# Kernel tuning notes

Hardware: AMD Instinct MI355X
Metric: run time of the kernel (lower is better)

Reference implementation:

```python
import jax, jax.numpy as jnp
import numpy as np


def _proj(W, b, x):
    # 1x1 conv == per-pixel GEMM over channels: [O,C] x [B,C,H,W] -> [B,O,H,W]
    return jnp.einsum('oc,bchw->bohw', W, x) + b[None, :, None, None]


def _cross(src, ctx, Wq, bq, Wk, bk, Wv, bv):
    # queries from src, keys/values from ctx; returns [B,C,H,W]
    B, C, H, W = src.shape
    HW = H * W
    q = _proj(Wq, bq, src).reshape(B, -1, HW)   # [B, C//8, HW]
    k = _proj(Wk, bk, ctx).reshape(B, -1, HW)   # [B, C//8, HW]
    v = _proj(Wv, bv, ctx).reshape(B, C, HW)    # [B, C,    HW]
    # attn[b,i,j] = softmax_j( q[b,:,i] . k[b,:,j] )
    attn = jax.nn.softmax(jnp.einsum('bci,bcj->bij', q, k), axis=-1)
    out = jnp.einsum('bcj,bij->bci', v, attn)   # [B, C, HW]
    return out.reshape(B, C, H, W)


def setup_inputs() -> dict:
    key = jax.random.key(0)
    ks = jax.random.split(key, 8)
    dim = 256
    B, H, W = 4, 64, 64
    return {
        'x': jax.random.normal(ks[0], (B, dim, H, W), jnp.float32),
        'y': jax.random.normal(ks[1], (B, dim, H, W), jnp.float32),
        'Wq': jax.random.normal(ks[2], (dim // 8, dim), jnp.float32) * 0.05,
        'bq': jax.random.normal(ks[3], (dim // 8,), jnp.float32) * 0.05,
        'Wk': jax.random.normal(ks[4], (dim // 8, dim), jnp.float32) * 0.05,
        'bk': jax.random.normal(ks[5], (dim // 8,), jnp.float32) * 0.05,
        'Wv': jax.random.normal(ks[6], (dim, dim), jnp.float32) * 0.05,
        'bv': jax.random.normal(ks[7], (dim,), jnp.float32) * 0.05,
    }


def reference(x, y, Wq, bq, Wk, bk, Wv, bv):
    outx = _cross(x, y, Wq, bq, Wk, bk, Wv, bv)  # x queries attend to y
    outy = _cross(y, x, Wq, bq, Wk, bk, Wv, bv)  # y queries attend to x
    return (outx, outy)
```

## Files before the change

### kernel.cpp

```cpp
#include <hip/hip_runtime.h>

#define BB 4
#define CC 256
#define DD 32
#define SS 4096

typedef __bf16 bf16;
typedef __bf16 bf16x8 __attribute__((ext_vector_type(8)));
typedef __bf16 bf16x4 __attribute__((ext_vector_type(4)));
typedef float f32x4 __attribute__((ext_vector_type(4)));
typedef unsigned int u32;
typedef unsigned short u16;

#define Q_OFF  0
#define K_OFF  1048576
#define V_OFF  2097152
#define WB_OFF 10485760

static __device__ __forceinline__ u32 pack2(float lo, float hi) {
    bf16 a = (bf16)lo, b = (bf16)hi;
    u16 ua = __builtin_bit_cast(u16, a), ub = __builtin_bit_cast(u16, b);
    return (u32)ua | ((u32)ub << 16);
}

__global__ __launch_bounds__(256) void convert_w_kernel(
    const float* __restrict__ Wq, const float* __restrict__ Wk,
    const float* __restrict__ Wv, bf16* __restrict__ wb)
{
    const int gid = blockIdx.x*256 + threadIdx.x;
    const int idx = gid*8;
    const int o = idx >> 8, cc = idx & 255;
    const float* row = (o < 32) ? (Wq + (size_t)o*CC)
                     : (o < 64) ? (Wk + (size_t)(o-32)*CC)
                                : (Wv + (size_t)(o-64)*CC);
    const float4 a = *(const float4*)(row + cc);
    const float4 c = *(const float4*)(row + cc + 4);
    bf16x8 pk;
    pk[0]=(bf16)a.x; pk[1]=(bf16)a.y; pk[2]=(bf16)a.z; pk[3]=(bf16)a.w;
    pk[4]=(bf16)c.x; pk[5]=(bf16)c.y; pk[6]=(bf16)c.z; pk[7]=(bf16)c.w;
    *(bf16x8*)(wb + idx) = pk;
}

__global__ __launch_bounds__(256, 2) void proj_all_kernel(
    const float* __restrict__ x, const float* __restrict__ y,
    const bf16* __restrict__ wb,
    const float* __restrict__ bq, const float* __restrict__ bk,
    const float* __restrict__ bv,
    bf16* __restrict__ qout, bf16* __restrict__ kout, bf16* __restrict__ vout)
{
    __shared__ __align__(16) char smem[2*5120];
    bf16* xT  = (bf16*)smem;
    u32*  xTw = (u32*)smem;

    const int t    = threadIdx.x;
    const int lane = t & 63;
    const int w    = t >> 6;
    const int ln   = lane & 15;
    const int quad = lane >> 4;

    const int bid  = blockIdx.x;
    const int dirb = bid & 7;
    const int src  = dirb >> 2;
    const int b    = dirb & 3;
    const int i0   = (bid >> 3) * 64;
    const float* in = src ? y : x;
    const float* xbase = in + (size_t)b*CC*SS + i0;

    const int cp = t >> 4;
    const int pq = (t & 15) * 4;

    float bias[5];
    #pragma unroll
    for (int nbl = 0; nbl < 5; ++nbl) {
        const int o = 80*w + nbl*16 + ln;
        bias[nbl] = (o < 32) ? bq[o] : (o < 64) ? bk[o-32] : bv[o-64];
    }
    f32x4 acc[4][5];
    #pragma unroll
    for (int mb = 0; mb < 4; ++mb)
        #pragma unroll
        for (int nbl = 0; nbl < 5; ++nbl)
            acc[mb][nbl] = (f32x4){bias[nbl], bias[nbl], bias[nbl], bias[nbl]};

    const bf16* wrow = wb + (size_t)(80*w + ln)*CC + quad*8;
    bf16x8 bf[5];
    #pragma unroll
    for (int nbl = 0; nbl < 5; ++nbl)
        bf[nbl] = *(const bf16x8*)(wrow + (size_t)nbl*16*CC);

    {
        const float* r0 = xbase + (size_t)(2*cp)*SS + pq;
        const float4 a0 = *(const float4*)r0;
        const float4 a1 = *(const float4*)(r0 + SS);
        xTw[(pq+0)*20 + cp] = pack2(a0.x, a1.x);
        xTw[(pq+1)*20 + cp] = pack2(a0.y, a1.y);
        xTw[(pq+2)*20 + cp] = pack2(a0.z, a1.z);
        xTw[(pq+3)*20 + cp] = pack2(a0.w, a1.w);
    }
    float4 a0, a1;
    {
        const float* r1 = xbase + (size_t)(32 + 2*cp)*SS + pq;
        a0 = *(const float4*)r1;
        a1 = *(const float4*)(r1 + SS);
    }
    __syncthreads();

    for (int n = 0; n < 8; ++n) {
        bf16x8 af[4];
        #pragma unroll
        for (int mb = 0; mb < 4; ++mb)
            af[mb] = *(const bf16x8*)(xT + (n&1)*2560 + (mb*16 + ln)*40 + quad*8);
        if (n < 7) {
            u32* dst = xTw + ((n+1)&1)*1280;
            dst[(pq+0)*20 + cp] = pack2(a0.x, a1.x);
            dst[(pq+1)*20 + cp] = pack2(a0.y, a1.y);
            dst[(pq+2)*20 + cp] = pack2(a0.z, a1.z);
            dst[(pq+3)*20 + cp] = pack2(a0.w, a1.w);
        }
        {
            const int cc2 = ((n+2)*32) & 255;
            const float* r2 = xbase + (size_t)(cc2 + 2*cp)*SS + pq;
            a0 = *(const float4*)r2;
            a1 = *(const float4*)(r2 + SS);
        }
        #pragma unroll
        for (int mb = 0; mb < 4; ++mb)
            #pragma unroll
            for (int nbl = 0; nbl < 5; ++nbl)
                acc[mb][nbl] = __builtin_amdgcn_mfma_f32_16x16x32_bf16(
                                   af[mb], bf[nbl], acc[mb][nbl], 0, 0, 0);
        const int ccn = ((n+1)*32) & 255;
        #pragma unroll
        for (int nbl = 0; nbl < 5; ++nbl)
            bf[nbl] = *(const bf16x8*)(wrow + (size_t)nbl*16*CC + ccn);
        __syncthreads();
    }

    bf16* qo = qout + (size_t)(src*BB + b)*SS*DD;
    bf16* ko = kout + (size_t)(src*BB + b)*SS*DD;
    bf16* vo = vout + (size_t)(src*BB + b)*CC*SS;
    #pragma unroll
    for (int nbl = 0; nbl < 5; ++nbl) {
        const int o = 80*w + nbl*16 + ln;
        if (o < 32) {
            #pragma unroll
            for (int mb = 0; mb < 4; ++mb)
                #pragma unroll
                for (int r = 0; r < 4; ++r)
                    qo[(size_t)(i0 + mb*16 + quad*4 + r)*DD + o] = (bf16)acc[mb][nbl][r];
        } else if (o < 64) {
            #pragma unroll
            for (int mb = 0; mb < 4; ++mb)
                #pragma unroll
                for (int r = 0; r < 4; ++r)
                    ko[(size_t)(i0 + mb*16 + quad*4 + r)*DD + (o-32)] = (bf16)acc[mb][nbl][r];
        } else {
            const int c = o - 64;
            #pragma unroll
            for (int mb = 0; mb < 4; ++mb) {
                bf16x4 pk;
                #pragma unroll
                for (int r = 0; r < 4; ++r) pk[r] = (bf16)acc[mb][nbl][r];
                *(bf16x4*)(vo + (size_t)c*SS + i0 + mb*16 + quad*4) = pk;
            }
        }
    }
}

#define SM_M 16.0f

__global__ __launch_bounds__(256, 2) void attn_kernel(
    const bf16* __restrict__ qg, const bf16* __restrict__ kg,
    const bf16* __restrict__ vg, float* __restrict__ out)
{
    __shared__ __align__(16) char smem[18688];
    bf16*  p_s = (bf16*)smem;
    float* l_s = (float*)(smem + 18432);

    const int t    = threadIdx.x;
    const int lane = t & 63;
    const int w    = t >> 6;
    const int ln   = lane & 15;
    const int quad = lane >> 4;

    const int bid  = blockIdx.x;
    const int dirb = bid & 7;
    const int dir  = dirb >> 2;
    const int b    = dirb & 3;
    const int i0   = (bid >> 3) * 64;

    const bf16* q = qg + ((size_t)dir*BB + b)*SS*DD + (size_t)i0*DD;
    const bf16* k = kg + ((size_t)(1-dir)*BB + b)*SS*DD;
    const bf16* v = vg + ((size_t)(1-dir)*BB + b)*CC*SS;
    float* op = out + ((size_t)dir*BB + b)*CC*SS;

    const bf16x8 b_q = *(const bf16x8*)(q + (size_t)(w*16 + ln)*DD + quad*8);
    const bf16* kbase = k + (size_t)ln*DD + quad*8;
    const bf16* vptr[4];
    #pragma unroll
    for (int cb = 0; cb < 4; ++cb)
        vptr[cb] = v + (size_t)(w*64 + cb*16 + ln)*SS + quad*8;

    f32x4 o[4][4];
    #pragma unroll
    for (int qb = 0; qb < 4; ++qb)
        #pragma unroll
        for (int cb = 0; cb < 4; ++cb) o[qb][cb] = (f32x4){0.f,0.f,0.f,0.f};
    float lp = 0.f;

    bf16x8 kf[4], vf[2][4];
    #pragma unroll
    for (int nb = 0; nb < 4; ++nb)
        kf[nb] = *(const bf16x8*)(kbase + (size_t)(nb*16)*DD);
    #pragma unroll
    for (int ks = 0; ks < 2; ++ks)
        #pragma unroll
        for (int cb = 0; cb < 4; ++cb)
            vf[ks][cb] = *(const bf16x8*)(vptr[cb] + ks*32);

    {
        f32x4 s[4];
        #pragma unroll
        for (int nb = 0; nb < 4; ++nb)
            s[nb] = __builtin_amdgcn_mfma_f32_16x16x32_bf16(
                        kf[nb], b_q, (f32x4){0.f,0.f,0.f,0.f}, 0, 0, 0);
        #pragma unroll
        for (int nb = 0; nb < 4; ++nb)
            kf[nb] = *(const bf16x8*)(kbase + (size_t)(64 + nb*16)*DD);
        #pragma unroll
        for (int nb = 0; nb < 4; ++nb) {
            bf16x4 pk;
            #pragma unroll
            for (int r = 0; r < 4; ++r) {
                const float e = __expf(fminf(s[nb][r] - SM_M, 60.0f));
                lp += e;
                pk[r] = (bf16)e;
            }
            *(bf16x4*)(p_s + (w*16 + ln)*72 + nb*16 + quad*4) = pk;
        }
    }

    for (int n = 0; n < 64; ++n) {
        __syncthreads();
        const bf16* pr = p_s + (n & 1)*4608;
        bf16* pw = p_s + ((n + 1) & 1)*4608;

        f32x4 s[4];
        if (n < 63) {
            #pragma unroll
            for (int nb = 0; nb < 4; ++nb)
                s[nb] = __builtin_amdgcn_mfma_f32_16x16x32_bf16(
                            kf[nb], b_q, (f32x4){0.f,0.f,0.f,0.f}, 0, 0, 0);
            const int j2 = ((n + 2) << 6) & (SS - 1);
            #pragma unroll
            for (int nb = 0; nb < 4; ++nb)
                kf[nb] = *(const bf16x8*)(kbase + (size_t)(j2 + nb*16)*DD);
        }

        #pragma unroll
        for (int ks = 0; ks < 2; ++ks) {
            bf16x8 ap[4];
            #pragma unroll
            for (int qb = 0; qb < 4; ++qb)
                ap[qb] = *(const bf16x8*)(pr + (qb*16 + ln)*72 + ks*32 + quad*8);
            #pragma unroll
            for (int qb = 0; qb < 4; ++qb)
                #pragma unroll
                for (int cb = 0; cb < 4; ++cb)
                    o[qb][cb] = __builtin_amdgcn_mfma_f32_16x16x32_bf16(
                                    ap[qb], vf[ks][cb], o[qb][cb], 0, 0, 0);
        }
        const int j1 = ((n + 1) << 6) & (SS - 1);
        #pragma unroll
        for (int ks = 0; ks < 2; ++ks)
            #pragma unroll
            for (int cb = 0; cb < 4; ++cb)
                vf[ks][cb] = *(const bf16x8*)(vptr[cb] + j1 + ks*32);

        if (n < 63) {
            #pragma unroll
            for (int nb = 0; nb < 4; ++nb) {
                bf16x4 pk;
                #pragma unroll
                for (int r = 0; r < 4; ++r) {
                    const float e = __expf(fminf(s[nb][r] - SM_M, 60.0f));
                    lp += e;
                    pk[r] = (bf16)e;
                }
                *(bf16x4*)(pw + (w*16 + ln)*72 + nb*16 + quad*4) = pk;
            }
        }
    }

    lp += __shfl_xor(lp, 16);
    lp += __shfl_xor(lp, 32);
    if (lane < 16) l_s[w*16 + ln] = lp;
    __syncthreads();

    #pragma unroll
    for (int qb = 0; qb < 4; ++qb) {
        const f32x4 lq = *(const f32x4*)(l_s + qb*16 + quad*4);
        const float ri0 = 1.0f/lq[0], ri1 = 1.0f/lq[1], ri2 = 1.0f/lq[2], ri3 = 1.0f/lq[3];
        #pragma unroll
        for (int cb = 0; cb < 4; ++cb) {
            const int c = w*64 + cb*16 + ln;
            float4 val = make_float4(o[qb][cb][0]*ri0, o[qb][cb][1]*ri1,
                                     o[qb][cb][2]*ri2, o[qb][cb][3]*ri3);
            *(float4*)(op + (size_t)c*SS + i0 + qb*16 + quad*4) = val;
        }
    }
}

extern "C" void kernel_launch(void* const* d_in, const int* in_sizes, int n_in,
                              void* d_out, int out_size, void* d_ws, size_t ws_size,
                              hipStream_t stream)
{
    const float* x  = (const float*)d_in[0];
    const float* y  = (const float*)d_in[1];
    const float* Wq = (const float*)d_in[2];
    const float* bq = (const float*)d_in[3];
    const float* Wk = (const float*)d_in[4];
    const float* bk = (const float*)d_in[5];
    const float* Wv = (const float*)d_in[6];
    const float* bv = (const float*)d_in[7];
    float* out = (float*)d_out;
    bf16* ws   = (bf16*)d_ws;

    bf16* qw = ws + Q_OFF;
    bf16* kw = ws + K_OFF;
    bf16* vw = ws + V_OFF;
    bf16* wb = ws + WB_OFF;

    convert_w_kernel<<<40,  256, 0, stream>>>(Wq, Wk, Wv, wb);
    proj_all_kernel <<<512, 256, 0, stream>>>(x, y, wb, bq, bk, bv, qw, kw, vw);
    attn_kernel     <<<512, 256, 0, stream>>>(qw, kw, vw, out);
}
```

Before: 253.6 us.

## Halve projection tile, swizzle LDS, and deepen attention K/V prefetch pipeline

The projection kernel now processes 32 pixels per block, so twice as many blocks launch and occupancy rises to four blocks per CU. Only half the threads stage input, and an XOR-swizzled LDS layout replaces the padded one. The attention kernel also swaps its padded P tile for an XOR-swizzled layout to avoid bank conflicts. It double-buffers K and V fragments in registers, prefetching one more iteration ahead and unrolling by two. This raises register pressure and reuses less weight data per pixel in the projection.

```diff
diff --git a/kernel.cpp b/kernel.cpp
--- a/kernel.cpp
+++ b/kernel.cpp
@@ -41,14 +41,14 @@
     *(bf16x8*)(wb + idx) = pk;
 }
 
-__global__ __launch_bounds__(256, 2) void proj_all_kernel(
+__global__ __launch_bounds__(256, 4) void proj_all_kernel(
     const float* __restrict__ x, const float* __restrict__ y,
     const bf16* __restrict__ wb,
     const float* __restrict__ bq, const float* __restrict__ bk,
     const float* __restrict__ bv,
     bf16* __restrict__ qout, bf16* __restrict__ kout, bf16* __restrict__ vout)
 {
-    __shared__ __align__(16) char smem[2*5120];
+    __shared__ __align__(16) char smem[2*4096];
     bf16* xT  = (bf16*)smem;
     u32*  xTw = (u32*)smem;
 
@@ -62,12 +62,13 @@
     const int dirb = bid & 7;
     const int src  = dirb >> 2;
     const int b    = dirb & 3;
-    const int i0   = (bid >> 3) * 64;
+    const int i0   = (bid >> 3) * 32;
     const float* in = src ? y : x;
     const float* xbase = in + (size_t)b*CC*SS + i0;
 
-    const int cp = t >> 4;
-    const int pq = (t & 15) * 4;
+    const bool stager = (t < 128);
+    const int cp = t >> 3;
+    const int pq = (t & 7) * 4;
 
     float bias[5];
     #pragma unroll
@@ -75,9 +76,9 @@
         const int o = 80*w + nbl*16 + ln;
         bias[nbl] = (o < 32) ? bq[o] : (o < 64) ? bk[o-32] : bv[o-64];
     }
-    f32x4 acc[4][5];
-    #pragma unroll
-    for (int mb = 0; mb < 4; ++mb)
+    f32x4 acc[2][5];
+    #pragma unroll
+    for (int mb = 0; mb < 2; ++mb)
         #pragma unroll
         for (int nbl = 0; nbl < 5; ++nbl)
             acc[mb][nbl] = (f32x4){bias[nbl], bias[nbl], bias[nbl], bias[nbl]};
@@ -88,43 +89,45 @@
     for (int nbl = 0; nbl < 5; ++nbl)
         bf[nbl] = *(const bf16x8*)(wrow + (size_t)nbl*16*CC);
 
-    {
+    float4 a0, a1;
+    if (stager) {
         const float* r0 = xbase + (size_t)(2*cp)*SS + pq;
-        const float4 a0 = *(const float4*)r0;
-        const float4 a1 = *(const float4*)(r0 + SS);
-        xTw[(pq+0)*20 + cp] = pack2(a0.x, a1.x);
-        xTw[(pq+1)*20 + cp] = pack2(a0.y, a1.y);
-        xTw[(pq+2)*20 + cp] = pack2(a0.z, a1.z);
-        xTw[(pq+3)*20 + cp] = pack2(a0.w, a1.w);
-    }
-    float4 a0, a1;
-    {
+        const float4 c0 = *(const float4*)r0;
+        const float4 c1 = *(const float4*)(r0 + SS);
+        const int chb = cp >> 2, lo = cp & 3;
+        xTw[(pq+0)*32 + ((chb ^ ((pq+0)&7)) << 2) + lo] = pack2(c0.x, c1.x);
+        xTw[(pq+1)*32 + ((chb ^ ((pq+1)&7)) << 2) + lo] = pack2(c0.y, c1.y);
+        xTw[(pq+2)*32 + ((chb ^ ((pq+2)&7)) << 2) + lo] = pack2(c0.z, c1.z);
+        xTw[(pq+3)*32 + ((chb ^ ((pq+3)&7)) << 2) + lo] = pack2(c0.w, c1.w);
         const float* r1 = xbase + (size_t)(32 + 2*cp)*SS + pq;
         a0 = *(const float4*)r1;
         a1 = *(const float4*)(r1 + SS);
     }
     __syncthreads();
 
+    const int swz = ln & 7;
     for (int n = 0; n < 8; ++n) {
-        bf16x8 af[4];
-        #pragma unroll
-        for (int mb = 0; mb < 4; ++mb)
-            af[mb] = *(const bf16x8*)(xT + (n&1)*2560 + (mb*16 + ln)*40 + quad*8);
-        if (n < 7) {
-            u32* dst = xTw + ((n+1)&1)*1280;
-            dst[(pq+0)*20 + cp] = pack2(a0.x, a1.x);
-            dst[(pq+1)*20 + cp] = pack2(a0.y, a1.y);
-            dst[(pq+2)*20 + cp] = pack2(a0.z, a1.z);
-            dst[(pq+3)*20 + cp] = pack2(a0.w, a1.w);
-        }
-        {
+        bf16x8 af[2];
+        #pragma unroll
+        for (int mb = 0; mb < 2; ++mb)
+            af[mb] = *(const bf16x8*)(xT + (n&1)*2048 + (mb*16 + ln)*64
+                                      + ((quad ^ swz) << 3));
+        if (n < 7 && stager) {
+            u32* dst = xTw + ((n+1)&1)*1024;
+            const int chb = cp >> 2, lo = cp & 3;
+            dst[(pq+0)*32 + ((chb ^ ((pq+0)&7)) << 2) + lo] = pack2(a0.x, a1.x);
+            dst[(pq+1)*32 + ((chb ^ ((pq+1)&7)) << 2) + lo] = pack2(a0.y, a1.y);
+            dst[(pq+2)*32 + ((chb ^ ((pq+2)&7)) << 2) + lo] = pack2(a0.z, a1.z);
+            dst[(pq+3)*32 + ((chb ^ ((pq+3)&7)) << 2) + lo] = pack2(a0.w, a1.w);
+        }
+        if (stager) {
             const int cc2 = ((n+2)*32) & 255;
             const float* r2 = xbase + (size_t)(cc2 + 2*cp)*SS + pq;
             a0 = *(const float4*)r2;
             a1 = *(const float4*)(r2 + SS);
         }
         #pragma unroll
-        for (int mb = 0; mb < 4; ++mb)
+        for (int mb = 0; mb < 2; ++mb)
             #pragma unroll
             for (int nbl = 0; nbl < 5; ++nbl)
                 acc[mb][nbl] = __builtin_amdgcn_mfma_f32_16x16x32_bf16(
@@ -144,20 +147,20 @@
         const int o = 80*w + nbl*16 + ln;
         if (o < 32) {
             #pragma unroll
-            for (int mb = 0; mb < 4; ++mb)
+            for (int mb = 0; mb < 2; ++mb)
                 #pragma unroll
                 for (int r = 0; r < 4; ++r)
                     qo[(size_t)(i0 + mb*16 + quad*4 + r)*DD + o] = (bf16)acc[mb][nbl][r];
         } else if (o < 64) {
             #pragma unroll
-            for (int mb = 0; mb < 4; ++mb)
+            for (int mb = 0; mb < 2; ++mb)
                 #pragma unroll
                 for (int r = 0; r < 4; ++r)
                     ko[(size_t)(i0 + mb*16 + quad*4 + r)*DD + (o-32)] = (bf16)acc[mb][nbl][r];
         } else {
             const int c = o - 64;
             #pragma unroll
-            for (int mb = 0; mb < 4; ++mb) {
+            for (int mb = 0; mb < 2; ++mb) {
                 bf16x4 pk;
                 #pragma unroll
                 for (int r = 0; r < 4; ++r) pk[r] = (bf16)acc[mb][nbl][r];
@@ -173,9 +176,9 @@
     const bf16* __restrict__ qg, const bf16* __restrict__ kg,
     const bf16* __restrict__ vg, float* __restrict__ out)
 {
-    __shared__ __align__(16) char smem[18688];
+    __shared__ __align__(16) char smem[16640];
     bf16*  p_s = (bf16*)smem;
-    float* l_s = (float*)(smem + 18432);
+    float* l_s = (float*)(smem + 16384);
 
     const int t    = threadIdx.x;
     const int lane = t & 63;
@@ -208,25 +211,33 @@
         for (int cb = 0; cb < 4; ++cb) o[qb][cb] = (f32x4){0.f,0.f,0.f,0.f};
     float lp = 0.f;
 
-    bf16x8 kf[4], vf[2][4];
-    #pragma unroll
-    for (int nb = 0; nb < 4; ++nb)
-        kf[nb] = *(const bf16x8*)(kbase + (size_t)(nb*16)*DD);
-    #pragma unroll
-    for (int ks = 0; ks < 2; ++ks)
-        #pragma unroll
-        for (int cb = 0; cb < 4; ++cb)
-            vf[ks][cb] = *(const bf16x8*)(vptr[cb] + ks*32);
-
+    const int swz  = ln & 7;
+    const int prow = (w*16 + ln)*64;
+
+    bf16x8 kfA[4], kfB[4], vfA[2][4], vfB[2][4];
     {
+        bf16x8 k0[4];
+        #pragma unroll
+        for (int nb = 0; nb < 4; ++nb)
+            k0[nb]  = *(const bf16x8*)(kbase + (size_t)(nb*16)*DD);
+        #pragma unroll
+        for (int nb = 0; nb < 4; ++nb)
+            kfB[nb] = *(const bf16x8*)(kbase + (size_t)(64  + nb*16)*DD);
+        #pragma unroll
+        for (int nb = 0; nb < 4; ++nb)
+            kfA[nb] = *(const bf16x8*)(kbase + (size_t)(128 + nb*16)*DD);
+        #pragma unroll
+        for (int ks = 0; ks < 2; ++ks)
+            #pragma unroll
+            for (int cb = 0; cb < 4; ++cb) {
+                vfA[ks][cb] = *(const bf16x8*)(vptr[cb] + ks*32);
+                vfB[ks][cb] = *(const bf16x8*)(vptr[cb] + 64 + ks*32);
+            }
         f32x4 s[4];
         #pragma unroll
         for (int nb = 0; nb < 4; ++nb)
             s[nb] = __builtin_amdgcn_mfma_f32_16x16x32_bf16(
-                        kf[nb], b_q, (f32x4){0.f,0.f,0.f,0.f}, 0, 0, 0);
-        #pragma unroll
-        for (int nb = 0; nb < 4; ++nb)
-            kf[nb] = *(const bf16x8*)(kbase + (size_t)(64 + nb*16)*DD);
+                        k0[nb], b_q, (f32x4){0.f,0.f,0.f,0.f}, 0, 0, 0);
         #pragma unroll
         for (int nb = 0; nb < 4; ++nb) {
             bf16x4 pk;
@@ -236,47 +247,45 @@
                 lp += e;
                 pk[r] = (bf16)e;
             }
-            *(bf16x4*)(p_s + (w*16 + ln)*72 + nb*16 + quad*4) = pk;
-        }
-    }
-
-    for (int n = 0; n < 64; ++n) {
+            *(bf16x4*)(p_s + prow + (((2*nb + (quad >> 1)) ^ swz) << 3)
+                       + (quad & 1)*4) = pk;
+        }
+    }
+
+    auto attn_iter = [&](int n, bf16x8 (&vfc)[2][4], bf16x8 (&kfu)[4],
+                         const bf16* pr, bf16* pw) {
         __syncthreads();
-        const bf16* pr = p_s + (n & 1)*4608;
-        bf16* pw = p_s + ((n + 1) & 1)*4608;
-
         f32x4 s[4];
         if (n < 63) {
             #pragma unroll
             for (int nb = 0; nb < 4; ++nb)
                 s[nb] = __builtin_amdgcn_mfma_f32_16x16x32_bf16(
-                            kf[nb], b_q, (f32x4){0.f,0.f,0.f,0.f}, 0, 0, 0);
-            const int j2 = ((n + 2) << 6) & (SS - 1);
+                            kfu[nb], b_q, (f32x4){0.f,0.f,0.f,0.f}, 0, 0, 0);
+            const int j3 = ((n + 3) << 6) & (SS - 1);
             #pragma unroll
             for (int nb = 0; nb < 4; ++nb)
-                kf[nb] = *(const bf16x8*)(kbase + (size_t)(j2 + nb*16)*DD);
-        }
-
+                kfu[nb] = *(const bf16x8*)(kbase + (size_t)(j3 + nb*16)*DD);
+        }
         #pragma unroll
         for (int ks = 0; ks < 2; ++ks) {
             bf16x8 ap[4];
             #pragma unroll
             for (int qb = 0; qb < 4; ++qb)
-                ap[qb] = *(const bf16x8*)(pr + (qb*16 + ln)*72 + ks*32 + quad*8);
+                ap[qb] = *(const bf16x8*)(pr + (qb*16 + ln)*64
+                                          + (((ks*4 + quad) ^ swz) << 3));
             #pragma unroll
             for (int qb = 0; qb < 4; ++qb)
                 #pragma unroll
                 for (int cb = 0; cb < 4; ++cb)
                     o[qb][cb] = __builtin_amdgcn_mfma_f32_16x16x32_bf16(
-                                    ap[qb], vf[ks][cb], o[qb][cb], 0, 0, 0);
-        }
-        const int j1 = ((n + 1) << 6) & (SS - 1);
+                                    ap[qb], vfc[ks][cb], o[qb][cb], 0, 0, 0);
+        }
+        const int j2 = ((n + 2) << 6) & (SS - 1);
         #pragma unroll
         for (int ks = 0; ks < 2; ++ks)
             #pragma unroll
             for (int cb = 0; cb < 4; ++cb)
-                vf[ks][cb] = *(const bf16x8*)(vptr[cb] + j1 + ks*32);
-
+                vfc[ks][cb] = *(const bf16x8*)(vptr[cb] + j2 + ks*32);
         if (n < 63) {
             #pragma unroll
             for (int nb = 0; nb < 4; ++nb) {
@@ -287,9 +296,15 @@
                     lp += e;
                     pk[r] = (bf16)e;
                 }
-                *(bf16x4*)(pw + (w*16 + ln)*72 + nb*16 + quad*4) = pk;
+                *(bf16x4*)(pw + prow + (((2*nb + (quad >> 1)) ^ swz) << 3)
+                           + (quad & 1)*4) = pk;
             }
         }
+    };
+
+    for (int n = 0; n < 64; n += 2) {
+        attn_iter(n,     vfA, kfB, p_s,        p_s + 4096);
+        attn_iter(n + 1, vfB, kfA, p_s + 4096, p_s);
     }
 
     lp += __shfl_xor(lp, 16);
@@ -331,7 +346,7 @@
     bf16* vw = ws + V_OFF;
     bf16* wb = ws + WB_OFF;
 
-    convert_w_kernel<<<40,  256, 0, stream>>>(Wq, Wk, Wv, wb);
-    proj_all_kernel <<<512, 256, 0, stream>>>(x, y, wb, bq, bk, bv, qw, kw, vw);
-    attn_kernel     <<<512, 256, 0, stream>>>(qw, kw, vw, out);
-}
+    convert_w_kernel<<<40,   256, 0, stream>>>(Wq, Wk, Wv, wb);
+    proj_all_kernel <<<1024, 256, 0, stream>>>(x, y, wb, bq, bk, bv, qw, kw, vw);
+    attn_kernel     <<<512,  256, 0, stream>>>(qw, kw, vw, out);
+}
```

Result: slower. 272.9 us (+7.6%).

## Deepen K/V register prefetch, swizzle P tile in LDS, use lighter barriers

Applied to the files above, without the earlier changes.

The attention loop is unrolled by two with ping-pong register buffers for K and V, so each global load is issued one iteration earlier than before. The P tile in LDS drops its padding in favour of an XOR swizzle on 8-element chunks, which shrinks shared memory while avoiding bank conflicts. The row-sum is kept as four separate partial sums to shorten the dependency chain, and __syncthreads is replaced by a barrier that waits only on LDS counters. The extra register buffers raise register pressure, which could hurt occupancy at two blocks per CU.

```diff
diff --git a/kernel.cpp b/kernel.cpp
--- a/kernel.cpp
+++ b/kernel.cpp
@@ -21,6 +21,12 @@
     bf16 a = (bf16)lo, b = (bf16)hi;
     u16 ua = __builtin_bit_cast(u16, a), ub = __builtin_bit_cast(u16, b);
     return (u32)ua | ((u32)ub << 16);
+}
+
+static __device__ __forceinline__ void bar_lds() {
+    asm volatile("s_waitcnt lgkmcnt(0)" ::: "memory");
+    __builtin_amdgcn_s_barrier();
+    asm volatile("" ::: "memory");
 }
 
 __global__ __launch_bounds__(256) void convert_w_kernel(
@@ -103,7 +109,7 @@
         a0 = *(const float4*)r1;
         a1 = *(const float4*)(r1 + SS);
     }
-    __syncthreads();
+    bar_lds();
 
     for (int n = 0; n < 8; ++n) {
         bf16x8 af[4];
@@ -133,7 +139,7 @@
         #pragma unroll
         for (int nbl = 0; nbl < 5; ++nbl)
             bf[nbl] = *(const bf16x8*)(wrow + (size_t)nbl*16*CC + ccn);
-        __syncthreads();
+        bar_lds();
     }
 
     bf16* qo = qout + (size_t)(src*BB + b)*SS*DD;
@@ -173,9 +179,9 @@
     const bf16* __restrict__ qg, const bf16* __restrict__ kg,
     const bf16* __restrict__ vg, float* __restrict__ out)
 {
-    __shared__ __align__(16) char smem[18688];
+    __shared__ __align__(16) char smem[16640];
     bf16*  p_s = (bf16*)smem;
-    float* l_s = (float*)(smem + 18432);
+    float* l_s = (float*)(smem + 16384);
 
     const int t    = threadIdx.x;
     const int lane = t & 63;
@@ -206,77 +212,83 @@
     for (int qb = 0; qb < 4; ++qb)
         #pragma unroll
         for (int cb = 0; cb < 4; ++cb) o[qb][cb] = (f32x4){0.f,0.f,0.f,0.f};
-    float lp = 0.f;
-
-    bf16x8 kf[4], vf[2][4];
-    #pragma unroll
-    for (int nb = 0; nb < 4; ++nb)
-        kf[nb] = *(const bf16x8*)(kbase + (size_t)(nb*16)*DD);
-    #pragma unroll
-    for (int ks = 0; ks < 2; ++ks)
-        #pragma unroll
-        for (int cb = 0; cb < 4; ++cb)
-            vf[ks][cb] = *(const bf16x8*)(vptr[cb] + ks*32);
-
+    f32x4 lpv = (f32x4){0.f,0.f,0.f,0.f};
+
+    const int swz  = ln & 7;
+    const int prow = (w*16 + ln)*64;
+
+    bf16x8 kfA[4], kfB[4], vfA[2][4], vfB[2][4];
     {
+        bf16x8 k0[4];
+        #pragma unroll
+        for (int nb = 0; nb < 4; ++nb)
+            k0[nb]  = *(const bf16x8*)(kbase + (size_t)(nb*16)*DD);
+        #pragma unroll
+        for (int nb = 0; nb < 4; ++nb)
+            kfB[nb] = *(const bf16x8*)(kbase + (size_t)(64  + nb*16)*DD);
+        #pragma unroll
+        for (int nb = 0; nb < 4; ++nb)
+            kfA[nb] = *(const bf16x8*)(kbase + (size_t)(128 + nb*16)*DD);
+        #pragma unroll
+        for (int ks = 0; ks < 2; ++ks)
+            #pragma unroll
+            for (int cb = 0; cb < 4; ++cb) {
+                vfA[ks][cb] = *(const bf16x8*)(vptr[cb] + ks*32);
+                vfB[ks][cb] = *(const bf16x8*)(vptr[cb] + 64 + ks*32);
+            }
         f32x4 s[4];
         #pragma unroll
         for (int nb = 0; nb < 4; ++nb)
             s[nb] = __builtin_amdgcn_mfma_f32_16x16x32_bf16(
-                        kf[nb], b_q, (f32x4){0.f,0.f,0.f,0.f}, 0, 0, 0);
-        #pragma unroll
-        for (int nb = 0; nb < 4; ++nb)
-            kf[nb] = *(const bf16x8*)(kbase + (size_t)(64 + nb*16)*DD);
+                        k0[nb], b_q, (f32x4){0.f,0.f,0.f,0.f}, 0, 0, 0);
         #pragma unroll
         for (int nb = 0; nb < 4; ++nb) {
             bf16x4 pk;
             #pragma unroll
             for (int r = 0; r < 4; ++r) {
                 const float e = __expf(fminf(s[nb][r] - SM_M, 60.0f));
-                lp += e;
+                lpv[r] += e;
                 pk[r] = (bf16)e;
             }
-            *(bf16x4*)(p_s + (w*16 + ln)*72 + nb*16 + quad*4) = pk;
-        }
-    }
-
-    for (int n = 0; n < 64; ++n) {
-        __syncthreads();
-        const bf16* pr = p_s + (n & 1)*4608;
-        bf16* pw = p_s + ((n + 1) & 1)*4608;
-
+            *(bf16x4*)(p_s + prow + (((2*nb + (quad >> 1)) ^ swz) << 3)
+                       + (quad & 1)*4) = pk;
+        }
+    }
+
+    auto attn_iter = [&](int n, bf16x8 (&vfc)[2][4], bf16x8 (&kfu)[4],
+                         const bf16* pr, bf16* pw) {
+        bar_lds();
         f32x4 s[4];
         if (n < 63) {
             #pragma unroll
             for (int nb = 0; nb < 4; ++nb)
                 s[nb] = __builtin_amdgcn_mfma_f32_16x16x32_bf16(
-                            kf[nb], b_q, (f32x4){0.f,0.f,0.f,0.f}, 0, 0, 0);
-            const int j2 = ((n + 2) << 6) & (SS - 1);
+                            kfu[nb], b_q, (f32x4){0.f,0.f,0.f,0.f}, 0, 0, 0);
+            const int j3 = ((n + 3) << 6) & (SS - 1);
             #pragma unroll
             for (int nb = 0; nb < 4; ++nb)
-                kf[nb] = *(const bf16x8*)(kbase + (size_t)(j2 + nb*16)*DD);
-        }
-
+                kfu[nb] = *(const bf16x8*)(kbase + (size_t)(j3 + nb*16)*DD);
+        }
         #pragma unroll
         for (int ks = 0; ks < 2; ++ks) {
             bf16x8 ap[4];
             #pragma unroll
             for (int qb = 0; qb < 4; ++qb)
-                ap[qb] = *(const bf16x8*)(pr + (qb*16 + ln)*72 + ks*32 + quad*8);
+                ap[qb] = *(const bf16x8*)(pr + (qb*16 + ln)*64
+                                          + (((ks*4 + quad) ^ swz) << 3));
             #pragma unroll
             for (int qb = 0; qb < 4; ++qb)
                 #pragma unroll
                 for (int cb = 0; cb < 4; ++cb)
                     o[qb][cb] = __builtin_amdgcn_mfma_f32_16x16x32_bf16(
-                                    ap[qb], vf[ks][cb], o[qb][cb], 0, 0, 0);
-        }
-        const int j1 = ((n + 1) << 6) & (SS - 1);
+                                    ap[qb], vfc[ks][cb], o[qb][cb], 0, 0, 0);
+        }
+        const int j2 = ((n + 2) << 6) & (SS - 1);
         #pragma unroll
         for (int ks = 0; ks < 2; ++ks)
             #pragma unroll
             for (int cb = 0; cb < 4; ++cb)
-                vf[ks][cb] = *(const bf16x8*)(vptr[cb] + j1 + ks*32);
-
+                vfc[ks][cb] = *(const bf16x8*)(vptr[cb] + j2 + ks*32);
         if (n < 63) {
             #pragma unroll
             for (int nb = 0; nb < 4; ++nb) {
@@ -284,14 +296,21 @@
                 #pragma unroll
                 for (int r = 0; r < 4; ++r) {
                     const float e = __expf(fminf(s[nb][r] - SM_M, 60.0f));
-                    lp += e;
+                    lpv[r] += e;
                     pk[r] = (bf16)e;
                 }
-                *(bf16x4*)(pw + (w*16 + ln)*72 + nb*16 + quad*4) = pk;
+                *(bf16x4*)(pw + prow + (((2*nb + (quad >> 1)) ^ swz) << 3)
+                           + (quad & 1)*4) = pk;
             }
         }
-    }
-
+    };
+
+    for (int n = 0; n < 64; n += 2) {
+        attn_iter(n,     vfA, kfB, p_s,        p_s + 4096);
+        attn_iter(n + 1, vfB, kfA, p_s + 4096, p_s);
+    }
+
+    float lp = (lpv[0] + lpv[1]) + (lpv[2] + lpv[3]);
     lp += __shfl_xor(lp, 16);
     lp += __shfl_xor(lp, 32);
     if (lane < 16) l_s[w*16 + ln] = lp;
```

Result: no change. 255.4 us (+0.7%).

## Replace per-iteration block barriers in attention with LDS flag handshakes and 4-slot P ring

Applied to the files above, without the earlier changes.

The attention kernel's per-iteration __syncthreads is replaced by per-slot LDS counters. Each wave increments a counter after writing its P tile and spins on it before reading. P becomes a 4-deep ring with an XOR-swizzled layout instead of padding, and S is computed two tiles ahead so waves can drift apart. It also switches to exp2f with a folded log2e, drops the clamp, adds s_setprio around the PV MFMAs, and uses a lighter lgkmcnt-only barrier in the projection kernel. This trades barrier stalls for spin-wait polling and doubles the LDS footprint, which may reduce occupancy.

```diff
diff --git a/kernel.cpp b/kernel.cpp
--- a/kernel.cpp
+++ b/kernel.cpp
@@ -21,6 +21,12 @@
     bf16 a = (bf16)lo, b = (bf16)hi;
     u16 ua = __builtin_bit_cast(u16, a), ub = __builtin_bit_cast(u16, b);
     return (u32)ua | ((u32)ub << 16);
+}
+
+static __device__ __forceinline__ void bar_lds() {
+    asm volatile("s_waitcnt lgkmcnt(0)" ::: "memory");
+    __builtin_amdgcn_s_barrier();
+    asm volatile("" ::: "memory");
 }
 
 __global__ __launch_bounds__(256) void convert_w_kernel(
@@ -103,7 +109,7 @@
         a0 = *(const float4*)r1;
         a1 = *(const float4*)(r1 + SS);
     }
-    __syncthreads();
+    bar_lds();
 
     for (int n = 0; n < 8; ++n) {
         bf16x8 af[4];
@@ -133,7 +139,7 @@
         #pragma unroll
         for (int nbl = 0; nbl < 5; ++nbl)
             bf[nbl] = *(const bf16x8*)(wrow + (size_t)nbl*16*CC + ccn);
-        __syncthreads();
+        bar_lds();
     }
 
     bf16* qo = qout + (size_t)(src*BB + b)*SS*DD;
@@ -167,15 +173,18 @@
     }
 }
 
-#define SM_M 16.0f
+#define SM_M  16.0f
+#define L2E   1.4426950408889634f
+#define SM_C  (SM_M * L2E)
 
 __global__ __launch_bounds__(256, 2) void attn_kernel(
     const bf16* __restrict__ qg, const bf16* __restrict__ kg,
     const bf16* __restrict__ vg, float* __restrict__ out)
 {
-    __shared__ __align__(16) char smem[18688];
+    __shared__ __align__(16) char smem[33056];
     bf16*  p_s = (bf16*)smem;
-    float* l_s = (float*)(smem + 18432);
+    float* l_s = (float*)(smem + 32768);
+    u32*   flg = (u32*)(smem + 33024);
 
     const int t    = threadIdx.x;
     const int lane = t & 63;
@@ -183,6 +192,8 @@
     const int ln   = lane & 15;
     const int quad = lane >> 4;
 
+    if (t < 8) flg[t] = 0;
+
     const int bid  = blockIdx.x;
     const int dirb = bid & 7;
     const int dir  = dirb >> 2;
@@ -206,7 +217,36 @@
     for (int qb = 0; qb < 4; ++qb)
         #pragma unroll
         for (int cb = 0; cb < 4; ++cb) o[qb][cb] = (f32x4){0.f,0.f,0.f,0.f};
-    float lp = 0.f;
+    f32x4 lpv = (f32x4){0.f,0.f,0.f,0.f};
+
+    const int swz  = ln & 7;
+    const int prow = (w*16 + ln)*64;
+
+    auto wait_ge = [&](u32* p, u32 tgt) {
+        while (__hip_atomic_load(p, __ATOMIC_RELAXED,
+                                 __HIP_MEMORY_SCOPE_WORKGROUP) < tgt)
+            __builtin_amdgcn_s_sleep(1);
+        asm volatile("" ::: "memory");
+    };
+    auto emit_p = [&](int slot, const f32x4* s) {
+        bf16* pw = p_s + slot*4096;
+        #pragma unroll
+        for (int nb = 0; nb < 4; ++nb) {
+            bf16x4 pk;
+            #pragma unroll
+            for (int r = 0; r < 4; ++r) {
+                const float e = exp2f(s[nb][r]*L2E - SM_C);
+                lpv[r] += e;
+                pk[r] = (bf16)e;
+            }
+            *(bf16x4*)(pw + prow + (((2*nb + (quad >> 1)) ^ swz) << 3)
+                       + (quad & 1)*4) = pk;
+        }
+        asm volatile("s_waitcnt lgkmcnt(0)" ::: "memory");
+        if (lane == 0)
+            __hip_atomic_fetch_add(&flg[slot], 1u, __ATOMIC_RELAXED,
+                                   __HIP_MEMORY_SCOPE_WORKGROUP);
+    };
 
     bf16x8 kf[4], vf[2][4];
     #pragma unroll
@@ -217,6 +257,8 @@
         #pragma unroll
         for (int cb = 0; cb < 4; ++cb)
             vf[ks][cb] = *(const bf16x8*)(vptr[cb] + ks*32);
+
+    __syncthreads();
 
     {
         f32x4 s[4];
@@ -227,42 +269,43 @@
         #pragma unroll
         for (int nb = 0; nb < 4; ++nb)
             kf[nb] = *(const bf16x8*)(kbase + (size_t)(64 + nb*16)*DD);
-        #pragma unroll
-        for (int nb = 0; nb < 4; ++nb) {
-            bf16x4 pk;
-            #pragma unroll
-            for (int r = 0; r < 4; ++r) {
-                const float e = __expf(fminf(s[nb][r] - SM_M, 60.0f));
-                lp += e;
-                pk[r] = (bf16)e;
-            }
-            *(bf16x4*)(p_s + (w*16 + ln)*72 + nb*16 + quad*4) = pk;
-        }
+        emit_p(0, s);
+        #pragma unroll
+        for (int nb = 0; nb < 4; ++nb)
+            s[nb] = __builtin_amdgcn_mfma_f32_16x16x32_bf16(
+                        kf[nb], b_q, (f32x4){0.f,0.f,0.f,0.f}, 0, 0, 0);
+        #pragma unroll
+        for (int nb = 0; nb < 4; ++nb)
+            kf[nb] = *(const bf16x8*)(kbase + (size_t)(128 + nb*16)*DD);
+        emit_p(1, s);
     }
 
     for (int n = 0; n < 64; ++n) {
-        __syncthreads();
-        const bf16* pr = p_s + (n & 1)*4608;
-        bf16* pw = p_s + ((n + 1) & 1)*4608;
-
+        const int sl = n & 3;
         f32x4 s[4];
-        if (n < 63) {
+        const int n2 = n + 2;
+        if (n < 62) {
+            wait_ge(&flg[4 + (n2 & 3)], (u32)((n2 >> 2) * 4));
             #pragma unroll
             for (int nb = 0; nb < 4; ++nb)
                 s[nb] = __builtin_amdgcn_mfma_f32_16x16x32_bf16(
                             kf[nb], b_q, (f32x4){0.f,0.f,0.f,0.f}, 0, 0, 0);
-            const int j2 = ((n + 2) << 6) & (SS - 1);
+            const int j3 = ((n + 3) << 6) & (SS - 1);
             #pragma unroll
             for (int nb = 0; nb < 4; ++nb)
-                kf[nb] = *(const bf16x8*)(kbase + (size_t)(j2 + nb*16)*DD);
-        }
-
+                kf[nb] = *(const bf16x8*)(kbase + (size_t)(j3 + nb*16)*DD);
+        }
+        wait_ge(&flg[sl], (u32)(((n >> 2) + 1) * 4));
+        const bf16* pr = p_s + sl*4096;
+
+        __builtin_amdgcn_s_setprio(1);
         #pragma unroll
         for (int ks = 0; ks < 2; ++ks) {
             bf16x8 ap[4];
             #pragma unroll
             for (int qb = 0; qb < 4; ++qb)
-                ap[qb] = *(const bf16x8*)(pr + (qb*16 + ln)*72 + ks*32 + quad*8);
+                ap[qb] = *(const bf16x8*)(pr + (qb*16 + ln)*64
+                                          + (((ks*4 + quad) ^ swz) << 3));
             #pragma unroll
             for (int qb = 0; qb < 4; ++qb)
                 #pragma unroll
@@ -270,6 +313,8 @@
                     o[qb][cb] = __builtin_amdgcn_mfma_f32_16x16x32_bf16(
                                     ap[qb], vf[ks][cb], o[qb][cb], 0, 0, 0);
         }
+        __builtin_amdgcn_s_setprio(0);
+
         const int j1 = ((n + 1) << 6) & (SS - 1);
         #pragma unroll
         for (int ks = 0; ks < 2; ++ks)
@@ -277,21 +322,16 @@
             for (int cb = 0; cb < 4; ++cb)
                 vf[ks][cb] = *(const bf16x8*)(vptr[cb] + j1 + ks*32);
 
-        if (n < 63) {
-            #pragma unroll
-            for (int nb = 0; nb < 4; ++nb) {
-                bf16x4 pk;
-                #pragma unroll
-                for (int r = 0; r < 4; ++r) {
-                    const float e = __expf(fminf(s[nb][r] - SM_M, 60.0f));
-                    lp += e;
-                    pk[r] = (bf16)e;
-                }
-                *(bf16x4*)(pw + (w*16 + ln)*72 + nb*16 + quad*4) = pk;
-            }
-        }
-    }
-
+        asm volatile("s_waitcnt lgkmcnt(0)" ::: "memory");
+        if (lane == 0)
+            __hip_atomic_fetch_add(&flg[4 + sl], 1u, __ATOMIC_RELAXED,
+                                   __HIP_MEMORY_SCOPE_WORKGROUP);
+
+        if (n < 62)
+            emit_p(n2 & 3, s);
+    }
+
+    float lp = (lpv[0] + lpv[1]) + (lpv[2] + lpv[3]);
     lp += __shfl_xor(lp, 16);
     lp += __shfl_xor(lp, 32);
     if (lane < 16) l_s[w*16 + ln] = lp;
```

After: 258.4 us. Within noise of the previous version (+1.9%).
